# Optimization experiments

Hardware: AMD Instinct MI355X
Metric: run time of the kernel (lower is better)

The kernel has to match this reference:

```python
import jax, jax.numpy as jnp
import numpy as np
from jax import lax

EPS = 1e-4       # BatchNorm eps from module
THRESHOLD = 0.0  # TernaryActive threshold (default)

B, C_IN, H, W = 16, 32, 256, 256
C_OUT, K, STRIDE, PAD = 32, 3, 1, 1


def setup_inputs() -> dict:
    key = jax.random.key(0)
    ks = jax.random.split(key, 7)
    x = jax.random.normal(ks[0], (B, C_IN, H, W), dtype=jnp.float32)
    bn_gamma = jax.random.normal(ks[1], (C_IN,), dtype=jnp.float32) * 0.1 + 1.0
    bn_beta = jax.random.normal(ks[2], (C_IN,), dtype=jnp.float32) * 0.1
    bn_mean = jax.random.normal(ks[3], (C_IN,), dtype=jnp.float32) * 0.1
    bn_var = jax.random.uniform(ks[4], (C_IN,), dtype=jnp.float32, minval=0.5, maxval=1.5)
    fan_in = C_IN * K * K
    bound = 1.0 / np.sqrt(fan_in)
    conv_w = jax.random.uniform(ks[5], (C_OUT, C_IN, K, K), dtype=jnp.float32, minval=-bound, maxval=bound)
    conv_b = jax.random.uniform(ks[6], (C_OUT,), dtype=jnp.float32, minval=-bound, maxval=bound)
    return {"x": x, "bn_gamma": bn_gamma, "bn_beta": bn_beta,
            "bn_mean": bn_mean, "bn_var": bn_var,
            "conv_w": conv_w, "conv_b": conv_b}


def _ternary(x):
    # torch: output[x >= thr] = 1, then output[x <= -thr] = -1 (le overrides ge)
    return jnp.where(x <= -THRESHOLD, -1.0,
                     jnp.where(x >= THRESHOLD, 1.0, 0.0)).astype(x.dtype)


def reference(x, bn_gamma, bn_beta, bn_mean, bn_var, conv_w, conv_b):
    # BatchNorm2d (inference form with running stats), per-channel over C
    inv = bn_gamma / jnp.sqrt(bn_var + EPS)
    xh = x * inv[None, :, None, None] + (bn_beta - bn_mean * inv)[None, :, None, None]
    # Ternary quantize {-1, 0, 1}
    q = _ternary(xh)
    # Conv2d 3x3, stride 1, pad 1 (NCHW / OIHW)
    y = lax.conv_general_dilated(q, conv_w, window_strides=(STRIDE, STRIDE),
                                 padding=[(PAD, PAD), (PAD, PAD)],
                                 dimension_numbers=("NCHW", "OIHW", "NCHW"))
    y = y + conv_b[None, :, None, None]
    # ReLU
    return jnp.maximum(y, 0.0)
```

## Files before the change

### kernel.cpp

```cpp
#include <hip/hip_runtime.h>


#define B_    16
#define H_    256
#define W_    256
#define SW    32
#define YC    16
#define ROWB  2304
#define NITEM 576

typedef __bf16 bf16x8 __attribute__((ext_vector_type(8)));
typedef float  f32x4  __attribute__((ext_vector_type(4)));
union FragCast { int4 i; bf16x8 b; };

__device__ __forceinline__ unsigned short f2bf(float f) {
    union { float f; unsigned u; } c; c.f = f;
    unsigned u = c.u;
    u += 0x7FFFu + ((u >> 16) & 1u);
    return (unsigned short)(u >> 16);
}

__device__ __forceinline__ unsigned short quant1(float v, float sc, float sh) {
    float xh = __fadd_rn(__fmul_rn(v, sc), sh);
    return (xh <= 0.0f) ? (unsigned short)0xBF80u
         : ((xh >= 0.0f) ? (unsigned short)0x3F80u : (unsigned short)0u);
}

__launch_bounds__(256, 4)
__global__ void tbconv_kernel(const float* __restrict__ x,
                              const float* __restrict__ bn_g,
                              const float* __restrict__ bn_b,
                              const float* __restrict__ bn_m,
                              const float* __restrict__ bn_v,
                              const float* __restrict__ conv_w,
                              const float* __restrict__ conv_b,
                              float* __restrict__ out)
{
    __shared__ __align__(16) unsigned char smem[18432];
    __shared__ float sScale[32], sShift[32];
    unsigned int*  sW = (unsigned int*)smem;
    unsigned char* sQ = smem;

    const int tid = threadIdx.x;
    const int bx  = blockIdx.x;
    const int strip = bx >> 8;
    const int b     = (bx >> 4) & 15;
    const int yc    = bx & 15;
    const int x0 = strip * SW;
    const int y0 = yc * YC;

    if (tid < 32) {
        float s = __fdiv_rn(bn_g[tid], __fsqrt_rn(__fadd_rn(bn_v[tid], 1e-4f)));
        sScale[tid] = s;
        sShift[tid] = __fsub_rn(bn_b[tid], __fmul_rn(bn_m[tid], s));
    }
    for (int j = tid; j < 4608; j += 256) {
        int cp = j & 15, co = (j >> 4) & 31, t = j >> 9;
        float w0 = conv_w[(co * 32 + 2 * cp)     * 9 + t];
        float w1 = conv_w[(co * 32 + 2 * cp + 1) * 9 + t];
        sW[j] = (unsigned)f2bf(w0) | ((unsigned)f2bf(w1) << 16);
    }
    __syncthreads();

    const float* lp[3];
    int   lw0[3], lw1[3];
    float lsc[3], lsh[3];
    bool  lxok[3];
    const bool lv2 = (tid < 64);
    #pragma unroll
    for (int j = 0; j < 3; ++j) {
        int i = tid + 256 * j; if (i >= NITEM) i = 0;
        int ci = i / 18, pr = i - 18 * ci;
        int gx = x0 - 2 + 2 * pr;
        bool xok = (gx >= 0) && (gx < W_);
        int gxc = (gx < 0) ? 0 : ((gx > 254) ? 254 : gx);
        lp[j]   = x + (((size_t)(b * 32 + ci)) << 16) + gxc;
        lxok[j] = xok;
        int hx0 = 2 * pr - 1, hx1 = 2 * pr;
        int hc0 = (hx0 < 0)  ? 34 : hx0;
        int hc1 = (hx1 > 33) ? 35 : hx1;
        int q = ci >> 3, cl = ci & 7;
        lw0[j] = ((hc0 * 4 + (q ^ ((hc0 >> 1) & 3))) << 4) + cl * 2;
        lw1[j] = ((hc1 * 4 + (q ^ ((hc1 >> 1) & 3))) << 4) + cl * 2;
        lsc[j] = sScale[ci]; lsh[j] = sShift[ci];
    }

    const int lane = tid & 63, wave = tid >> 6;
    const int quad = lane >> 4, n = lane & 15;
    const int ct = wave >> 1, xh = wave & 1;
    const int xl = xh * 16 + n;

    FragCast fA[9];
    #pragma unroll
    for (int t = 0; t < 9; ++t)
        fA[t].i = *(const int4*)((const char*)sW + ((t * 32 + ct * 16 + n) * 32 + quad * 8) * 2);

    int dsoff[3];
    #pragma unroll
    for (int kw = 0; kw < 3; ++kw) {
        int hx = xl + kw;
        dsoff[kw] = (hx * 4 + (quad ^ ((hx >> 1) & 3))) << 4;
    }

    float bias[4];
    #pragma unroll
    for (int r = 0; r < 4; ++r)
        bias[r] = conv_b[ct * 16 + quad * 4 + r];
    const size_t obase = (((size_t)(b * 32 + ct * 16 + quad * 4)) << 16)
                       + ((size_t)y0 << 8) + (x0 + xl);

    __syncthreads();

    float2 v[3];
    auto load_row = [&](int gy) {
        bool yok = ((unsigned)gy < (unsigned)H_);
        #pragma unroll
        for (int j = 0; j < 3; ++j) {
            v[j] = make_float2(0.f, 0.f);
            if (yok && (j < 2 || lv2))
                v[j] = *(const float2*)(lp[j] + (gy << 8));
        }
    };
    auto scatter = [&](int gy, int slot) {
        bool yok = ((unsigned)gy < (unsigned)H_);
        char* rowp = (char*)sQ + slot * ROWB;
        #pragma unroll
        for (int j = 0; j < 3; ++j) {
            if (j < 2 || lv2) {
                unsigned short q0 = 0, q1 = 0;
                if (yok && lxok[j]) {
                    q0 = quant1(v[j].x, lsc[j], lsh[j]);
                    q1 = quant1(v[j].y, lsc[j], lsh[j]);
                }
                *(unsigned short*)(rowp + lw0[j]) = q0;
                *(unsigned short*)(rowp + lw1[j]) = q1;
            }
        }
    };

    load_row(y0 - 1); scatter(y0 - 1, 3);
    load_row(y0);     scatter(y0,     0);
    load_row(y0 + 1); scatter(y0 + 1, 1);
    load_row(y0 + 2);
    __syncthreads();

    for (int t8 = 0; t8 < YC / 4; ++t8) {
        #pragma unroll
        for (int u = 0; u < 4; ++u) {
            const int yy = t8 * 4 + u;
            const int y  = y0 + yy;

            f32x4 acc[3];
            #pragma unroll
            for (int kh = 0; kh < 3; ++kh) {
                const int sb = ((u + 3 + kh) & 3) * ROWB;
                f32x4 a = {0.f, 0.f, 0.f, 0.f};
                #pragma unroll
                for (int kw = 0; kw < 3; ++kw) {
                    FragCast fB;
                    fB.i = *(const int4*)((const char*)sQ + sb + dsoff[kw]);
                    a = __builtin_amdgcn_mfma_f32_16x16x32_bf16(fA[kh * 3 + kw].b, fB.b, a, 0, 0, 0);
                }
                acc[kh] = a;
            }

            if (yy <= YC - 2) scatter(y + 2, (u + 2) & 3);
            __syncthreads();

            #pragma unroll
            for (int r = 0; r < 4; ++r) {
                float s = __fadd_rn(__fadd_rn(acc[0][r], acc[1][r]),
                                    __fadd_rn(acc[2][r], bias[r]));
                out[obase + ((size_t)r << 16) + (yy << 8)] = fmaxf(s, 0.f);
            }
            if (yy <= YC - 3) load_row(y + 3);
        }
    }
}

extern "C" void kernel_launch(void* const* d_in, const int* in_sizes, int n_in,
                              void* d_out, int out_size, void* d_ws, size_t ws_size,
                              hipStream_t stream) {
    const float* x     = (const float*)d_in[0];
    const float* gamma = (const float*)d_in[1];
    const float* beta  = (const float*)d_in[2];
    const float* mean  = (const float*)d_in[3];
    const float* var   = (const float*)d_in[4];
    const float* w     = (const float*)d_in[5];
    const float* bias  = (const float*)d_in[6];
    float* o = (float*)d_out;

    dim3 grid(B_ * 8 * (H_ / YC));
    dim3 block(256);
    hipLaunchKernelGGL(tbconv_kernel, grid, block, 0, stream,
                       x, gamma, beta, mean, var, w, bias, o);
}
```

Before: 292.4 us.

## Process two output rows per step with 8-slot ring and taller row chunks

Each block now covers 32 output rows instead of 16, which halves the halo-row reloads and the per-block weight setup. The shared-memory row ring grows from 4 to 8 slots, and each iteration computes two output rows, so each B fragment loaded from LDS feeds MFMAs for both rows. This halves the number of barriers per output row, and global loads are prefetched two rows ahead. The grid shrinks to 1024 blocks, which may lower occupancy and tail balance, and the extra accumulators and prefetch registers raise register pressure.

```diff
diff --git a/kernel.cpp b/kernel.cpp
--- a/kernel.cpp
+++ b/kernel.cpp
@@ -5,7 +5,7 @@
 #define H_    256
 #define W_    256
 #define SW    32
-#define YC    16
+#define YC    32
 #define ROWB  2304
 #define NITEM 576
 
@@ -43,9 +43,9 @@
 
     const int tid = threadIdx.x;
     const int bx  = blockIdx.x;
-    const int strip = bx >> 8;
-    const int b     = (bx >> 4) & 15;
-    const int yc    = bx & 15;
+    const int strip = bx >> 7;
+    const int b     = (bx >> 3) & 15;
+    const int yc    = bx & 7;
     const int x0 = strip * SW;
     const int y0 = yc * YC;
 
@@ -111,17 +111,16 @@
 
     __syncthreads();
 
-    float2 v[3];
-    auto load_row = [&](int gy) {
+    auto load_row = [&](float2 (&dv)[3], int gy) {
         bool yok = ((unsigned)gy < (unsigned)H_);
         #pragma unroll
         for (int j = 0; j < 3; ++j) {
-            v[j] = make_float2(0.f, 0.f);
+            dv[j] = make_float2(0.f, 0.f);
             if (yok && (j < 2 || lv2))
-                v[j] = *(const float2*)(lp[j] + (gy << 8));
+                dv[j] = *(const float2*)(lp[j] + (gy << 8));
         }
     };
-    auto scatter = [&](int gy, int slot) {
+    auto scatter = [&](const float2 (&sv)[3], int gy, int slot) {
         bool yok = ((unsigned)gy < (unsigned)H_);
         char* rowp = (char*)sQ + slot * ROWB;
         #pragma unroll
@@ -129,8 +128,8 @@
             if (j < 2 || lv2) {
                 unsigned short q0 = 0, q1 = 0;
                 if (yok && lxok[j]) {
-                    q0 = quant1(v[j].x, lsc[j], lsh[j]);
-                    q1 = quant1(v[j].y, lsc[j], lsh[j]);
+                    q0 = quant1(sv[j].x, lsc[j], lsh[j]);
+                    q1 = quant1(sv[j].y, lsc[j], lsh[j]);
                 }
                 *(unsigned short*)(rowp + lw0[j]) = q0;
                 *(unsigned short*)(rowp + lw1[j]) = q1;
@@ -138,42 +137,67 @@
         }
     };
 
-    load_row(y0 - 1); scatter(y0 - 1, 3);
-    load_row(y0);     scatter(y0,     0);
-    load_row(y0 + 1); scatter(y0 + 1, 1);
-    load_row(y0 + 2);
+    float2 v[2][3];
+    {
+        float2 p0[3], p1[3], p2[3], p3[3];
+        load_row(p0, y0 - 1); load_row(p1, y0);
+        load_row(p2, y0 + 1); load_row(p3, y0 + 2);
+        load_row(v[0], y0 + 3); load_row(v[1], y0 + 4);
+        scatter(p0, y0 - 1, 7); scatter(p1, y0, 0);
+        scatter(p2, y0 + 1, 1); scatter(p3, y0 + 2, 2);
+    }
     __syncthreads();
 
-    for (int t8 = 0; t8 < YC / 4; ++t8) {
+    for (int t4 = 0; t4 < 4; ++t4) {
         #pragma unroll
         for (int u = 0; u < 4; ++u) {
-            const int yy = t8 * 4 + u;
+            const int yy = t4 * 8 + u * 2;
             const int y  = y0 + yy;
 
-            f32x4 acc[3];
+            if (yy <= 28) {
+                scatter(v[0], y + 3, (2 * u + 3) & 7);
+                scatter(v[1], y + 4, (2 * u + 4) & 7);
+            }
+            __syncthreads();
+
+            if (yy <= 26) {
+                load_row(v[0], y + 5);
+                load_row(v[1], y + 6);
+            }
+
+            f32x4 aA[3], aB[3];
             #pragma unroll
             for (int kh = 0; kh < 3; ++kh) {
-                const int sb = ((u + 3 + kh) & 3) * ROWB;
-                f32x4 a = {0.f, 0.f, 0.f, 0.f};
+                aA[kh] = (f32x4){0.f, 0.f, 0.f, 0.f};
+                aB[kh] = (f32x4){0.f, 0.f, 0.f, 0.f};
+            }
+            #pragma unroll
+            for (int j = 0; j < 4; ++j) {
+                const int sb = ((2 * u + 7 + j) & 7) * ROWB;
+                FragCast fB[3];
+                #pragma unroll
+                for (int kw = 0; kw < 3; ++kw)
+                    fB[kw].i = *(const int4*)((const char*)sQ + sb + dsoff[kw]);
                 #pragma unroll
                 for (int kw = 0; kw < 3; ++kw) {
-                    FragCast fB;
-                    fB.i = *(const int4*)((const char*)sQ + sb + dsoff[kw]);
-                    a = __builtin_amdgcn_mfma_f32_16x16x32_bf16(fA[kh * 3 + kw].b, fB.b, a, 0, 0, 0);
+                    if (j < 3)
+                        aA[j] = __builtin_amdgcn_mfma_f32_16x16x32_bf16(
+                                    fA[j * 3 + kw].b, fB[kw].b, aA[j], 0, 0, 0);
+                    if (j >= 1)
+                        aB[j - 1] = __builtin_amdgcn_mfma_f32_16x16x32_bf16(
+                                    fA[(j - 1) * 3 + kw].b, fB[kw].b, aB[j - 1], 0, 0, 0);
                 }
-                acc[kh] = a;
-            }
-
-            if (yy <= YC - 2) scatter(y + 2, (u + 2) & 3);
-            __syncthreads();
+            }
 
             #pragma unroll
             for (int r = 0; r < 4; ++r) {
-                float s = __fadd_rn(__fadd_rn(acc[0][r], acc[1][r]),
-                                    __fadd_rn(acc[2][r], bias[r]));
-                out[obase + ((size_t)r << 16) + (yy << 8)] = fmaxf(s, 0.f);
-            }
-            if (yy <= YC - 3) load_row(y + 3);
+                float sA = __fadd_rn(__fadd_rn(aA[0][r], aA[1][r]),
+                                     __fadd_rn(aA[2][r], bias[r]));
+                out[obase + ((size_t)r << 16) + ((size_t)yy << 8)] = fmaxf(sA, 0.f);
+                float sB = __fadd_rn(__fadd_rn(aB[0][r], aB[1][r]),
+                                     __fadd_rn(aB[2][r], bias[r]));
+                out[obase + ((size_t)r << 16) + ((size_t)(yy + 1) << 8)] = fmaxf(sB, 0.f);
+            }
         }
     }
 }
```

Result: no change. 290.9 us (-0.5%).

## Give each wave a private LDS ring and drop per-row block barriers

Applied to the files above, without the earlier changes.

Each wave now owns its own 4-row LDS ring of quantized input for its 16-column strip, so the per-row __syncthreads is removed and waves run independently. Tiles become 32 rows tall, with a two-deep register double buffer that prefetches global rows ahead of the scatter and MFMA work. Out-of-range pixels use NaN scale/shift so they quantize to zero without branches. The cost is that the two waves sharing a column strip each load and quantize the same input, doubling input traffic and quantization work, and the grid shrinks to half as many blocks.

```diff
diff --git a/kernel.cpp b/kernel.cpp
--- a/kernel.cpp
+++ b/kernel.cpp
@@ -4,10 +4,8 @@
 #define B_    16
 #define H_    256
 #define W_    256
-#define SW    32
-#define YC    16
-#define ROWB  2304
-#define NITEM 576
+#define ROWB  1280
+#define WLDS  (4 * ROWB)
 
 typedef __bf16 bf16x8 __attribute__((ext_vector_type(8)));
 typedef float  f32x4  __attribute__((ext_vector_type(4)));
@@ -36,18 +34,16 @@
                               const float* __restrict__ conv_b,
                               float* __restrict__ out)
 {
-    __shared__ __align__(16) unsigned char smem[18432];
+    __shared__ __align__(16) unsigned char smem[4 * WLDS];
     __shared__ float sScale[32], sShift[32];
-    unsigned int*  sW = (unsigned int*)smem;
-    unsigned char* sQ = smem;
+    unsigned int* sW = (unsigned int*)smem;
 
     const int tid = threadIdx.x;
     const int bx  = blockIdx.x;
-    const int strip = bx >> 8;
-    const int b     = (bx >> 4) & 15;
-    const int yc    = bx & 15;
-    const int x0 = strip * SW;
-    const int y0 = yc * YC;
+    const int strip = bx >> 7;
+    const int b     = (bx >> 3) & 15;
+    const int yc    = bx & 7;
+    const int y0    = yc * 32;
 
     if (tid < 32) {
         float s = __fdiv_rn(bn_g[tid], __fsqrt_rn(__fadd_rn(bn_v[tid], 1e-4f)));
@@ -62,118 +58,119 @@
     }
     __syncthreads();
 
-    const float* lp[3];
-    int   lw0[3], lw1[3];
-    float lsc[3], lsh[3];
-    bool  lxok[3];
-    const bool lv2 = (tid < 64);
-    #pragma unroll
-    for (int j = 0; j < 3; ++j) {
-        int i = tid + 256 * j; if (i >= NITEM) i = 0;
-        int ci = i / 18, pr = i - 18 * ci;
-        int gx = x0 - 2 + 2 * pr;
-        bool xok = (gx >= 0) && (gx < W_);
-        int gxc = (gx < 0) ? 0 : ((gx > 254) ? 254 : gx);
-        lp[j]   = x + (((size_t)(b * 32 + ci)) << 16) + gxc;
-        lxok[j] = xok;
-        int hx0 = 2 * pr - 1, hx1 = 2 * pr;
-        int hc0 = (hx0 < 0)  ? 34 : hx0;
-        int hc1 = (hx1 > 33) ? 35 : hx1;
-        int q = ci >> 3, cl = ci & 7;
-        lw0[j] = ((hc0 * 4 + (q ^ ((hc0 >> 1) & 3))) << 4) + cl * 2;
-        lw1[j] = ((hc1 * 4 + (q ^ ((hc1 >> 1) & 3))) << 4) + cl * 2;
-        lsc[j] = sScale[ci]; lsh[j] = sShift[ci];
-    }
-
     const int lane = tid & 63, wave = tid >> 6;
-    const int quad = lane >> 4, n = lane & 15;
-    const int ct = wave >> 1, xh = wave & 1;
-    const int xl = xh * 16 + n;
+    const int oct = lane >> 4, n = lane & 15;
+    const int xh = wave >> 1, ct = wave & 1;
+    const int x0w = strip * 32 + xh * 16;
 
     FragCast fA[9];
     #pragma unroll
     for (int t = 0; t < 9; ++t)
-        fA[t].i = *(const int4*)((const char*)sW + ((t * 32 + ct * 16 + n) * 32 + quad * 8) * 2);
+        fA[t].i = *(const int4*)((const char*)smem +
+                                 ((t * 32 + ct * 16 + n) * 32 + oct * 8) * 2);
 
+    unsigned loff[5], lwp[5];
+    float lsc[5], lsh[5];
+    #pragma unroll
+    for (int j = 0; j < 5; ++j) {
+        int i = lane + 64 * j;
+        int ci = i / 10, pr = i - 10 * ci;
+        int gx = x0w - 2 + 2 * pr;
+        bool xok = (gx >= 0) && (gx <= 254);
+        int gxc = (gx < 0) ? 0 : ((gx > 254) ? 254 : gx);
+        loff[j] = ((unsigned)(b * 32 + ci) << 18) + (unsigned)gxc * 4u;
+        int hx0 = 2 * pr - 1, hx1 = 2 * pr;
+        int hc0 = (hx0 < 0)  ? 18 : hx0;
+        int hc1 = (hx1 > 17) ? 19 : hx1;
+        int q = ci >> 3, cl = ci & 7;
+        unsigned w0 = (unsigned)(((hc0 * 4 + (q ^ ((hc0 >> 1) & 3))) << 4) + cl * 2);
+        unsigned w1 = (unsigned)(((hc1 * 4 + (q ^ ((hc1 >> 1) & 3))) << 4) + cl * 2);
+        lwp[j] = w0 | (w1 << 16);
+        float sc = sScale[ci], sh = sShift[ci];
+        if (!xok) { sc = __int_as_float(0x7FC00000); sh = sc; }
+        lsc[j] = sc; lsh[j] = sh;
+    }
+
+    char* ringp = (char*)smem + wave * WLDS;
     int dsoff[3];
     #pragma unroll
     for (int kw = 0; kw < 3; ++kw) {
-        int hx = xl + kw;
-        dsoff[kw] = (hx * 4 + (quad ^ ((hx >> 1) & 3))) << 4;
+        int hx = n + kw;
+        dsoff[kw] = (hx * 4 + (oct ^ ((hx >> 1) & 3))) << 4;
     }
 
     float bias[4];
     #pragma unroll
     for (int r = 0; r < 4; ++r)
-        bias[r] = conv_b[ct * 16 + quad * 4 + r];
-    const size_t obase = (((size_t)(b * 32 + ct * 16 + quad * 4)) << 16)
-                       + ((size_t)y0 << 8) + (x0 + xl);
+        bias[r] = conv_b[ct * 16 + oct * 4 + r];
+    const size_t obase = (((size_t)(b * 32 + ct * 16 + oct * 4)) << 16)
+                       + ((size_t)y0 << 8) + (x0w + n);
 
     __syncthreads();
 
-    float2 v[3];
-    auto load_row = [&](int gy) {
-        bool yok = ((unsigned)gy < (unsigned)H_);
+    const char* xb = (const char*)x;
+    auto load_row = [&](float2 (&dv)[5], int gy) {
+        const bool yok = ((unsigned)gy < (unsigned)H_);
+        const float nf = __int_as_float(0x7FC00000);
         #pragma unroll
-        for (int j = 0; j < 3; ++j) {
-            v[j] = make_float2(0.f, 0.f);
-            if (yok && (j < 2 || lv2))
-                v[j] = *(const float2*)(lp[j] + (gy << 8));
+        for (int j = 0; j < 5; ++j) {
+            dv[j] = make_float2(nf, nf);
+            if (yok) dv[j] = *(const float2*)(xb + loff[j] + ((unsigned)gy << 10));
         }
     };
-    auto scatter = [&](int gy, int slot) {
-        bool yok = ((unsigned)gy < (unsigned)H_);
-        char* rowp = (char*)sQ + slot * ROWB;
+    auto scatter = [&](const float2 (&sv)[5], int slot) {
+        char* rowp = ringp + slot * ROWB;
         #pragma unroll
-        for (int j = 0; j < 3; ++j) {
-            if (j < 2 || lv2) {
-                unsigned short q0 = 0, q1 = 0;
-                if (yok && lxok[j]) {
-                    q0 = quant1(v[j].x, lsc[j], lsh[j]);
-                    q1 = quant1(v[j].y, lsc[j], lsh[j]);
-                }
-                *(unsigned short*)(rowp + lw0[j]) = q0;
-                *(unsigned short*)(rowp + lw1[j]) = q1;
-            }
+        for (int j = 0; j < 5; ++j) {
+            unsigned short q0 = quant1(sv[j].x, lsc[j], lsh[j]);
+            unsigned short q1 = quant1(sv[j].y, lsc[j], lsh[j]);
+            *(unsigned short*)(rowp + (lwp[j] & 0xFFFFu)) = q0;
+            *(unsigned short*)(rowp + (lwp[j] >> 16))     = q1;
         }
     };
 
-    load_row(y0 - 1); scatter(y0 - 1, 3);
-    load_row(y0);     scatter(y0,     0);
-    load_row(y0 + 1); scatter(y0 + 1, 1);
-    load_row(y0 + 2);
-    __syncthreads();
+    float2 buf0[5], buf1[5];
+    load_row(buf0, y0 - 1);
+    load_row(buf1, y0);
+    scatter(buf0, 3);
+    scatter(buf1, 0);
+    load_row(buf1, y0 + 1);
 
-    for (int t8 = 0; t8 < YC / 4; ++t8) {
+    for (int t8 = 0; t8 < 8; ++t8) {
         #pragma unroll
         for (int u = 0; u < 4; ++u) {
-            const int yy = t8 * 4 + u;
-            const int y  = y0 + yy;
+            const int y  = t8 * 4 + u;
+            const int gy = y0 + y;
+
+            if (y <= 30) {
+                if ((u & 1) == 0) load_row(buf0, gy + 2);
+                else              load_row(buf1, gy + 2);
+            }
+            if ((u & 1) == 0) scatter(buf1, (u + 1) & 3);
+            else              scatter(buf0, (u + 1) & 3);
 
             f32x4 acc[3];
             #pragma unroll
             for (int kh = 0; kh < 3; ++kh) {
                 const int sb = ((u + 3 + kh) & 3) * ROWB;
+                FragCast fB[3];
+                #pragma unroll
+                for (int kw = 0; kw < 3; ++kw)
+                    fB[kw].i = *(const int4*)(ringp + sb + dsoff[kw]);
                 f32x4 a = {0.f, 0.f, 0.f, 0.f};
                 #pragma unroll
-                for (int kw = 0; kw < 3; ++kw) {
-                    FragCast fB;
-                    fB.i = *(const int4*)((const char*)sQ + sb + dsoff[kw]);
-                    a = __builtin_amdgcn_mfma_f32_16x16x32_bf16(fA[kh * 3 + kw].b, fB.b, a, 0, 0, 0);
-                }
+                for (int kw = 0; kw < 3; ++kw)
+                    a = __builtin_amdgcn_mfma_f32_16x16x32_bf16(
+                            fA[kh * 3 + kw].b, fB[kw].b, a, 0, 0, 0);
                 acc[kh] = a;
             }
-
-            if (yy <= YC - 2) scatter(y + 2, (u + 2) & 3);
-            __syncthreads();
 
             #pragma unroll
             for (int r = 0; r < 4; ++r) {
                 float s = __fadd_rn(__fadd_rn(acc[0][r], acc[1][r]),
                                     __fadd_rn(acc[2][r], bias[r]));
-                out[obase + ((size_t)r << 16) + (yy << 8)] = fmaxf(s, 0.f);
+                out[obase + ((size_t)r << 16) + ((size_t)y << 8)] = fmaxf(s, 0.f);
             }
-            if (yy <= YC - 3) load_row(y + 3);
         }
     }
 }
@@ -190,7 +187,7 @@
     const float* bias  = (const float*)d_in[6];
     float* o = (float*)d_out;
 
-    dim3 grid(B_ * 8 * (H_ / YC));
+    dim3 grid(B_ * 8 * 8);
     dim3 block(256);
     hipLaunchKernelGGL(tbconv_kernel, grid, block, 0, stream,
                        x, gamma, beta, mean, var, w, bias, o);
```

After: 410.3 us. 40.3% more time.
